# Kernel optimization log

Hardware: AMD Instinct MI355X
Metric: run time of the kernel (lower is better)

## Reference

```python
import jax, jax.numpy as jnp
import numpy as np

B, S, D, DEPTH = 2, 2048, 1024, 4
NUM_LEAVES = 2 ** DEPTH          # 16
NUM_DEC = NUM_LEAVES - 1         # 15


def setup_inputs() -> dict:
    key = jax.random.key(0)
    k1, k2, k3, k4, k5 = jax.random.split(key, 5)
    scale = 1.0 / np.sqrt(D)
    return {
        "x": jax.random.normal(k1, (B, S, D), dtype=jnp.float32),
        "dec_w": jax.random.normal(k2, (NUM_DEC, D), dtype=jnp.float32) * scale,
        "dec_b": jax.random.normal(k3, (NUM_DEC,), dtype=jnp.float32) * scale,
        "leaf_w": jax.random.normal(k4, (NUM_LEAVES, D, D), dtype=jnp.float32) * scale,  # [leaf, out, in] (torch Linear layout)
        "leaf_b": jax.random.normal(k5, (NUM_LEAVES, D), dtype=jnp.float32) * scale,
    }


def reference(x, dec_w, dec_b, leaf_w, leaf_b):
    num_leaves = leaf_w.shape[0]
    num_dec = num_leaves - 1
    # All decision-node sigmoids in one batched GEMM: [B,S,num_dec]
    dec = jax.nn.sigmoid(jnp.einsum("bsd,nd->bsn", x, dec_w) + dec_b)
    # Faithful to the original: each tree slot is multiplied exactly once by its
    # direct parent's decision (left child: p, right child: 1-p).
    leaf_idx = np.arange(num_dec, 2 * num_leaves - 1)      # slots holding leaf probs
    parent = (leaf_idx - 1) // 2                           # [num_leaves]
    is_left = (leaf_idx % 2 == 1)                          # [num_leaves]
    dec_p = dec[..., parent]                               # [B,S,num_leaves]
    leaf_probs = jnp.where(jnp.asarray(is_left), dec_p, 1.0 - dec_p)
    # All leaf MLPs as one batched GEMM: [B,S,L,D]
    leaf_out = jnp.einsum("bsd,lod->bslo", x, leaf_w) + leaf_b
    # Probability-weighted sum over leaves -> [B,S,D]
    return jnp.einsum("bslo,bsl->bso", leaf_out, leaf_probs)
```

## Files before the change

kernel.cpp:

```cpp
#include <hip/hip_runtime.h>
#include <stdint.h>


#define M_TOK 4096
#define DDIM  1024
#define KFLAT 9216

typedef __bf16 bf16x8 __attribute__((ext_vector_type(8)));
typedef float  f32x4  __attribute__((ext_vector_type(4)));
typedef unsigned short u16x4 __attribute__((ext_vector_type(4)));
typedef unsigned short u16x8 __attribute__((ext_vector_type(8)));

#define GLB(p) ((const __attribute__((address_space(1))) void*)(p))
#define LDS(p) ((__attribute__((address_space(3))) void*)(p))

__device__ __forceinline__ unsigned short f2bf(float f) {
    union { float f; uint32_t u; } v; v.f = f;
    uint32_t u = v.u;
    return (unsigned short)((u + 0x7fffu + ((u >> 16) & 1u)) >> 16);
}

__device__ __forceinline__ bf16x8 asbf(f32x4 v) {
    bf16x8 r; __builtin_memcpy(&r, &v, 16); return r;
}

template<int OFF>
__device__ __forceinline__ f32x4 dsr(uint32_t a) {
    f32x4 r;
    asm volatile("ds_read_b128 %0, %1 offset:%c2" : "=v"(r) : "v"(a), "i"(OFF));
    return r;
}

__global__ __launch_bounds__(256) void prep_dec_kernel(
    const float* __restrict__ x, const float* __restrict__ dec_w,
    const float* __restrict__ dec_b, const float* __restrict__ lw,
    const float* __restrict__ lb, unsigned short* __restrict__ wp,
    float* __restrict__ bw, unsigned short* __restrict__ xs,
    float* __restrict__ pmat)
{
    if (blockIdx.x < 1024) {
        int idx = blockIdx.x * 256 + threadIdx.x;
        int o  = idx >> 8;
        int k4 = (idx & 255) << 2;
        size_t src = (size_t)o * DDIM + k4;
        size_t dstb = (size_t)o * KFLAT + k4;
        float4 acc = make_float4(0.f, 0.f, 0.f, 0.f);
#pragma unroll
        for (int j = 0; j < 8; ++j) {
            const float4 a = *(const float4*)(lw + (size_t)(2*j)   * DDIM*DDIM + src);
            const float4 b = *(const float4*)(lw + (size_t)(2*j+1) * DDIM*DDIM + src);
            u16x4 d;
            d[0] = f2bf(a.x - b.x); d[1] = f2bf(a.y - b.y);
            d[2] = f2bf(a.z - b.z); d[3] = f2bf(a.w - b.w);
            *(u16x4*)(wp + dstb + (size_t)j * DDIM) = d;
            acc.x += b.x; acc.y += b.y; acc.z += b.z; acc.w += b.w;
        }
        u16x4 s;
        s[0] = f2bf(acc.x); s[1] = f2bf(acc.y); s[2] = f2bf(acc.z); s[3] = f2bf(acc.w);
        *(u16x4*)(wp + dstb + (size_t)8 * DDIM) = s;
        if ((idx & 255) == 0) {
            float sb = 0.f;
#pragma unroll
            for (int j = 0; j < 8; ++j) {
                float ba = lb[(2*j) * DDIM + o];
                float bb = lb[(2*j+1) * DDIM + o];
                bw[j * DDIM + o] = ba - bb;
                sb += bb;
            }
            bw[8 * DDIM + o] = sb;
        }
    } else {
        int m    = (blockIdx.x - 1024) * 4 + (threadIdx.x >> 6);
        int lane = threadIdx.x & 63;
        const float* xr = x + (size_t)m * DDIM + lane * 16;
        float xv[16];
        *(float4*)&xv[0]  = *(const float4*)(xr + 0);
        *(float4*)&xv[4]  = *(const float4*)(xr + 4);
        *(float4*)&xv[8]  = *(const float4*)(xr + 8);
        *(float4*)&xv[12] = *(const float4*)(xr + 12);
        float s[8];
#pragma unroll
        for (int j = 0; j < 8; ++j) {
            const float* wr = dec_w + (size_t)(7 + j) * DDIM + lane * 16;
            float a = 0.f;
#pragma unroll
            for (int i = 0; i < 16; i += 4) {
                float4 wv = *(const float4*)(wr + i);
                a = fmaf(xv[i], wv.x, fmaf(xv[i+1], wv.y, fmaf(xv[i+2], wv.z, fmaf(xv[i+3], wv.w, a))));
            }
            s[j] = a;
        }
#pragma unroll
        for (int j = 0; j < 8; ++j)
#pragma unroll
            for (int off = 32; off > 0; off >>= 1)
                s[j] += __shfl_xor(s[j], off);
        float p[8];
#pragma unroll
        for (int j = 0; j < 8; ++j)
            p[j] = 1.0f / (1.0f + expf(-(s[j] + dec_b[7 + j])));
        if (lane == 0) {
#pragma unroll
            for (int j = 0; j < 8; ++j)
                pmat[(size_t)m * 8 + j] = p[j];
        }
#pragma unroll
        for (int j = 0; j < 9; ++j) {
            float pj = (j < 8) ? p[j] : 1.0f;
            unsigned short* dst = xs + (size_t)m * KFLAT + j * DDIM + lane * 16;
#pragma unroll
            for (int c = 0; c < 2; ++c) {
                u16x8 o;
#pragma unroll
                for (int e = 0; e < 8; ++e) o[e] = f2bf(pj * xv[c * 8 + e]);
                *(u16x8*)(dst + c * 8) = o;
            }
        }
    }
}

#define WAITV8 asm volatile("s_waitcnt vmcnt(8)" ::: "memory")
#define WAITV4 asm volatile("s_waitcnt vmcnt(4)" ::: "memory")
#define WAITV0 asm volatile("s_waitcnt vmcnt(0)" ::: "memory")
#define BARR   __builtin_amdgcn_s_barrier()
#define LGKM0  do { asm volatile("s_waitcnt lgkmcnt(0)" ::: "memory"); \
                    __builtin_amdgcn_sched_barrier(0); } while(0)
#define LGKM4  do { asm volatile("s_waitcnt lgkmcnt(4)" ::: "memory"); \
                    __builtin_amdgcn_sched_barrier(0); } while(0)

#define MFMA_Q(q, SET) do { \
    __builtin_amdgcn_s_setprio(1); \
    _Pragma("unroll") \
    for (int mfl = 0; mfl < 2; ++mfl) { \
        _Pragma("unroll") \
        for (int j = 0; j < 4; ++j) { \
            acc[2*(q)+mfl][j] = __builtin_amdgcn_mfma_f32_16x16x32_bf16(asbf(SET[mfl][0]), asbf(bv[j][0]), acc[2*(q)+mfl][j], 0, 0, 0); \
            acc[2*(q)+mfl][j] = __builtin_amdgcn_mfma_f32_16x16x32_bf16(asbf(SET[mfl][1]), asbf(bv[j][1]), acc[2*(q)+mfl][j], 0, 0, 0); \
        } \
    } \
    __builtin_amdgcn_s_setprio(0); \
} while(0)

#define READ_A(SET, q) do { \
    SET[0][0] = dsr<(2*(q)+0)*2048>(bA0); \
    SET[0][1] = dsr<(2*(q)+0)*2048>(bA1); \
    SET[1][0] = dsr<(2*(q)+1)*2048>(bA0); \
    SET[1][1] = dsr<(2*(q)+1)*2048>(bA1); \
} while(0)

#define READ_B() do { \
    bv[0][0] = dsr<0*2048>(bB0); bv[0][1] = dsr<0*2048>(bB1); \
    bv[1][0] = dsr<1*2048>(bB0); bv[1][1] = dsr<1*2048>(bB1); \
    bv[2][0] = dsr<2*2048>(bB0); bv[2][1] = dsr<2*2048>(bB1); \
    bv[3][0] = dsr<3*2048>(bB0); bv[3][1] = dsr<3*2048>(bB1); \
} while(0)

__global__ __launch_bounds__(512, 2) void tree_gemm5(
    const unsigned short* __restrict__ xs,
    const unsigned short* __restrict__ wp,
    float* __restrict__ out, float* __restrict__ parts,
    int KG)
{
    extern __shared__ char smem[];
    const int tid  = threadIdx.x;
    const int lane = tid & 63;
    const int w    = tid >> 6;
    const int wm   = w >> 2, wn = w & 3;
    const int ra   = lane & 15;
    const int g16  = lane >> 4;

    const int bx  = blockIdx.x;
    const int xcd = bx & 7, ii = bx >> 3;
    const int nt  = xcd >> 1;
    const int mt  = (xcd & 1) * 8 + ii;
    const int m0  = mt * 256, n0 = nt * 256;
    const int g   = blockIdx.y;
    const int k0  = g * KG;
    const int NT  = KG >> 6;

    uint32_t sbase = (uint32_t)(uintptr_t)(__attribute__((address_space(3))) char*)smem;
    const uint32_t colb0 = (uint32_t)((g16 ^ (ra & 7)) << 4);
    const uint32_t colb1 = colb0 ^ 64;
    const uint32_t baseA0s = sbase + wm * 16384 + ra * 128 + colb0;
    const uint32_t baseA1s = sbase + wm * 16384 + ra * 128 + colb1;
    const uint32_t baseB0s = sbase + 65536 + wn * 8192 + ra * 128 + colb0;
    const uint32_t baseB1s = sbase + 65536 + wn * 8192 + ra * 128 + colb1;

    const int kel = (((lane & 7) ^ (lane >> 3)) & 7) * 8;
    const int rA  = w * 8 + (lane >> 3);

    auto stageA = [&](int buf, int tt, int hh) {
        const unsigned short* s0 = xs + (size_t)(m0 + hh * 128 + rA) * KFLAT + (k0 + tt * 64 + kel);
        char* d0 = smem + buf * 32768 + hh * 16384 + w * 1024;
        __builtin_amdgcn_global_load_lds(GLB(s0), LDS(d0), 16, 0, 0);
        __builtin_amdgcn_global_load_lds(GLB(s0 + (size_t)64 * KFLAT), LDS(d0 + 8192), 16, 0, 0);
    };
    auto stageB = [&](int buf, int tt, int hh) {
        const unsigned short* s0 = wp + (size_t)(n0 + hh * 128 + rA) * KFLAT + (k0 + tt * 64 + kel);
        char* d0 = smem + 65536 + buf * 32768 + hh * 16384 + w * 1024;
        __builtin_amdgcn_global_load_lds(GLB(s0), LDS(d0), 16, 0, 0);
        __builtin_amdgcn_global_load_lds(GLB(s0 + (size_t)64 * KFLAT), LDS(d0 + 8192), 16, 0, 0);
    };

    f32x4 acc[8][4] = {};
    f32x4 avA[2][2], avB[2][2], bv[4][2];

    stageA(0, 0, 0); stageA(0, 0, 1);
    stageB(0, 0, 0); stageB(0, 0, 1);
    stageA(1, 1, 0); stageA(1, 1, 1);
    stageB(1, 1, 0); stageB(1, 1, 1);
    WAITV8;
    BARR;

    int bt = 0, bt2 = 2;
    for (int t = 0; t < NT; ++t) {
        if (t) {
            if (t == NT - 1) { WAITV0; } else { WAITV4; }
            BARR;
        }
        if (t + 1 < NT) { stageA((t + 1) & 1, t + 1, 0); stageA((t + 1) & 1, t + 1, 1); }
        if (t + 2 < NT) { stageB(bt2, t + 2, 0); stageB(bt2, t + 2, 1); }

        const uint32_t aoff = (uint32_t)(t & 1) << 15;
        const uint32_t boff = (uint32_t)bt << 15;
        const uint32_t bA0 = baseA0s + aoff, bA1 = baseA1s + aoff;
        const uint32_t bB0 = baseB0s + boff, bB1 = baseB1s + boff;

        READ_B();
        READ_A(avA, 0);
        READ_A(avB, 1);
        LGKM4;  MFMA_Q(0, avA);
        READ_A(avA, 2);
        LGKM4;  MFMA_Q(1, avB);
        READ_A(avB, 3);
        LGKM4;  MFMA_Q(2, avA);
        LGKM0;  MFMA_Q(3, avB);

        bt  = (bt  == 2) ? 0 : bt  + 1;
        bt2 = (bt2 == 2) ? 0 : bt2 + 1;
    }

    float* dst = (g == 0) ? out : parts + (size_t)(g - 1) * M_TOK * DDIM;
#pragma unroll
    for (int mf = 0; mf < 8; ++mf)
#pragma unroll
        for (int e = 0; e < 4; ++e) {
            int row = m0 + wm * 128 + mf * 16 + g16 * 4 + e;
#pragma unroll
            for (int j = 0; j < 4; ++j)
                dst[(size_t)row * DDIM + n0 + wn * 64 + j * 16 + ra] = acc[mf][j][e];
        }
}

#define READ_AV4(q, b) do { \
    avA[0][0] = dsr<(b)*32768 + (2*(q)+0)*2048>(baseA0); \
    avA[0][1] = dsr<(b)*32768 + (2*(q)+0)*2048>(baseA1); \
    avA[1][0] = dsr<(b)*32768 + (2*(q)+1)*2048>(baseA0); \
    avA[1][1] = dsr<(b)*32768 + (2*(q)+1)*2048>(baseA1); \
} while(0)

#define READ_BV4(b) do { \
    bv[0][0] = dsr<(b)*32768 + 0*2048>(baseB0); bv[0][1] = dsr<(b)*32768 + 0*2048>(baseB1); \
    bv[1][0] = dsr<(b)*32768 + 1*2048>(baseB0); bv[1][1] = dsr<(b)*32768 + 1*2048>(baseB1); \
    bv[2][0] = dsr<(b)*32768 + 2*2048>(baseB0); bv[2][1] = dsr<(b)*32768 + 2*2048>(baseB1); \
    bv[3][0] = dsr<(b)*32768 + 3*2048>(baseB0); bv[3][1] = dsr<(b)*32768 + 3*2048>(baseB1); \
} while(0)

__global__ __launch_bounds__(512, 2) void tree_gemm4(
    const unsigned short* __restrict__ xs, const unsigned short* __restrict__ wp,
    float* __restrict__ out, float* __restrict__ parts, int KG)
{
    extern __shared__ char smem[];
    const int tid  = threadIdx.x;
    const int lane = tid & 63;
    const int w    = tid >> 6;
    const int wm   = w >> 2, wn = w & 3;
    const int ra   = lane & 15;
    const int g16  = lane >> 4;
    const int bx  = blockIdx.x;
    const int xcd = bx & 7, ii = bx >> 3;
    const int nt  = xcd >> 1;
    const int mt  = (xcd & 1) * 8 + ii;
    const int m0  = mt * 256, n0 = nt * 256;
    const int g   = blockIdx.y;
    const int k0  = g * KG;
    const int NI  = KG >> 7;
    uint32_t sbase = (uint32_t)(uintptr_t)(__attribute__((address_space(3))) char*)smem;
    const uint32_t colb0 = (uint32_t)((g16 ^ (ra & 7)) << 4);
    const uint32_t colb1 = colb0 ^ 64;
    const uint32_t baseA0 = sbase + wm * 16384 + ra * 128 + colb0;
    const uint32_t baseA1 = sbase + wm * 16384 + ra * 128 + colb1;
    const uint32_t baseB0 = sbase + 65536 + wn * 8192 + ra * 128 + colb0;
    const uint32_t baseB1 = sbase + 65536 + wn * 8192 + ra * 128 + colb1;
    const int kel = (((lane & 7) ^ (lane >> 3)) & 7) * 8;
    const int rA  = w * 8 + (lane >> 3);
    auto stageA = [&](int buf, int tt, int hh) {
        const unsigned short* s0 = xs + (size_t)(m0 + hh * 128 + rA) * KFLAT + (k0 + tt * 64 + kel);
        char* d0 = smem + buf * 32768 + hh * 16384 + w * 1024;
        __builtin_amdgcn_global_load_lds(GLB(s0), LDS(d0), 16, 0, 0);
        __builtin_amdgcn_global_load_lds(GLB(s0 + (size_t)64 * KFLAT), LDS(d0 + 8192), 16, 0, 0);
    };
    auto stageB = [&](int buf, int tt, int hh) {
        const unsigned short* s0 = wp + (size_t)(n0 + hh * 128 + rA) * KFLAT + (k0 + tt * 64 + kel);
        char* d0 = smem + 65536 + buf * 32768 + hh * 16384 + w * 1024;
        __builtin_amdgcn_global_load_lds(GLB(s0), LDS(d0), 16, 0, 0);
        __builtin_amdgcn_global_load_lds(GLB(s0 + (size_t)64 * KFLAT), LDS(d0 + 8192), 16, 0, 0);
    };
    f32x4 acc[8][4] = {};
    f32x4 avA[2][2], bv[4][2];
    stageA(0, 0, 0); stageA(0, 0, 1);
    stageB(0, 0, 0); stageB(0, 0, 1);
    stageB(1, 1, 0); stageB(1, 1, 1);
    WAITV4; BARR;
    for (int i = 0; i < NI; ++i) {
        const int t = 2 * i;
        const bool on = (i + 1 < NI);
        READ_BV4(0); READ_AV4(0, 0);
        stageA(1, t + 1, 0); stageA(1, t + 1, 1);
        BARR; LGKM0; MFMA_Q(0, avA); BARR;
        READ_AV4(1, 0); if (on) stageB(0, t + 2, 0);
        BARR; LGKM0; MFMA_Q(1, avA); BARR;
        READ_AV4(2, 0); if (on) stageB(0, t + 2, 1);
        BARR; LGKM0; MFMA_Q(2, avA); BARR;
        READ_AV4(3, 0);
        BARR; LGKM0; MFMA_Q(3, avA);
        if (on) { WAITV4; } else { WAITV0; }
        BARR;
        READ_BV4(1); READ_AV4(0, 1);
        if (on) { stageA(0, t + 2, 0); stageA(0, t + 2, 1); }
        BARR; LGKM0; MFMA_Q(0, avA); BARR;
        READ_AV4(1, 1); if (on) stageB(1, t + 3, 0);
        BARR; LGKM0; MFMA_Q(1, avA); BARR;
        READ_AV4(2, 1); if (on) stageB(1, t + 3, 1);
        BARR; LGKM0; MFMA_Q(2, avA); BARR;
        READ_AV4(3, 1);
        BARR; LGKM0; MFMA_Q(3, avA);
        if (on) WAITV4;
        BARR;
    }
    float* dst = (g == 0) ? out : parts + (size_t)(g - 1) * M_TOK * DDIM;
#pragma unroll
    for (int mf = 0; mf < 8; ++mf)
#pragma unroll
        for (int e = 0; e < 4; ++e) {
            int row = m0 + wm * 128 + mf * 16 + g16 * 4 + e;
#pragma unroll
            for (int j = 0; j < 4; ++j)
                dst[(size_t)row * DDIM + n0 + wn * 64 + j * 16 + ra] = acc[mf][j][e];
        }
}

__global__ __launch_bounds__(256) void reduce2_kernel(
    float* __restrict__ out, const float* __restrict__ parts,
    const float* __restrict__ pmat, const float* __restrict__ bw, int np)
{
    size_t i = (size_t)blockIdx.x * 256 + threadIdx.x;
    int m   = (int)(i >> 8);
    int col = (int)(i & 255) * 4;
    float4 a = ((const float4*)out)[i];
    for (int p = 0; p < np; ++p) {
        float4 b = ((const float4*)(parts + (size_t)p * M_TOK * DDIM))[i];
        a.x += b.x; a.y += b.y; a.z += b.z; a.w += b.w;
    }
    float4 pa = *(const float4*)(pmat + (size_t)m * 8);
    float4 pb = *(const float4*)(pmat + (size_t)m * 8 + 4);
    float4 bias = *(const float4*)(bw + 8 * DDIM + col);
#pragma unroll
    for (int l = 0; l < 8; ++l) {
        float pl = (l < 4) ? ((const float*)&pa)[l] : ((const float*)&pb)[l - 4];
        float4 bl = *(const float4*)(bw + l * DDIM + col);
        bias.x = fmaf(pl, bl.x, bias.x); bias.y = fmaf(pl, bl.y, bias.y);
        bias.z = fmaf(pl, bl.z, bias.z); bias.w = fmaf(pl, bl.w, bias.w);
    }
    a.x += bias.x; a.y += bias.y; a.z += bias.z; a.w += bias.w;
    ((float4*)out)[i] = a;
}

__global__ __launch_bounds__(256, 4) void tree_gemm3(
    const unsigned short* __restrict__ xs, const unsigned short* __restrict__ wp,
    const float* __restrict__ bw, const float* __restrict__ pmat,
    float* __restrict__ out, float* __restrict__ parts, int KG)
{
    __shared__ __align__(16) unsigned short Asm[2][128 * 32];
    __shared__ __align__(16) unsigned short Bsm[2][128 * 32];
    const int tid  = threadIdx.x;
    const int lane = tid & 63;
    const int w    = tid >> 6;
    const int wm   = w >> 1, wn = w & 1;
    const int bx   = blockIdx.x;
    const int xcd  = bx & 7;
    const int ii   = bx >> 3;
    const int mt   = xcd * 4 + (ii >> 3);
    const int nt   = ii & 7;
    const int m0   = mt * 128, n0 = nt * 128;
    const int g    = blockIdx.y;
    const int k0   = g * KG;
    const int ra   = lane & 15;
    const int kb   = (lane >> 4) * 8;
    f32x4 acc[4][4] = {};
    auto stage = [&](int buf, int t) {
#pragma unroll
        for (int c = 0; c < 2; ++c) {
            int row = w * 32 + c * 16 + (lane >> 2);
            int ke  = k0 + t * 32 + (lane & 3) * 8;
            const unsigned short* ga = xs + (size_t)(m0 + row) * KFLAT + ke;
            __builtin_amdgcn_global_load_lds(GLB(ga), LDS(&Asm[buf][w * 1024 + c * 512]), 16, 0, 0);
            const unsigned short* gb = wp + (size_t)(n0 + row) * KFLAT + ke;
            __builtin_amdgcn_global_load_lds(GLB(gb), LDS(&Bsm[buf][w * 1024 + c * 512]), 16, 0, 0);
// ... 58 lines not shown
{
    size_t i = (size_t)blockIdx.x * 256 + threadIdx.x;
    float4 a = ((const float4*)out)[i];
    for (int p = 0; p < np; ++p) {
        float4 b = ((const float4*)(parts + (size_t)p * M_TOK * DDIM))[i];
        a.x += b.x; a.y += b.y; a.z += b.z; a.w += b.w;
    }
    ((float4*)out)[i] = a;
}

extern "C" void kernel_launch(void* const* d_in, const int* in_sizes, int n_in,
                              void* d_out, int out_size, void* d_ws, size_t ws_size,
                              hipStream_t stream) {
    (void)in_sizes; (void)n_in; (void)out_size;
    const float* x     = (const float*)d_in[0];
    const float* dec_w = (const float*)d_in[1];
    const float* dec_b = (const float*)d_in[2];
    const float* lw    = (const float*)d_in[3];
    const float* lb    = (const float*)d_in[4];
    float* out = (float*)d_out;
    uint8_t* w8 = (uint8_t*)d_ws;

    unsigned short* xs   = (unsigned short*)(w8);
    unsigned short* wp   = (unsigned short*)(w8 + 75497472);
    float*          bw   = (float*)(w8 + 94371840);
    float*          pmat = (float*)(w8 + 94408704);
    float*          parts= (float*)(w8 + 94539776);
    const size_t NEED3 = 94539776 + 2ull * 16777216;
    const size_t NEED4 = 94539776 + 3ull * 16777216;

    int ks = (ws_size >= NEED4) ? 4 : (ws_size >= NEED3) ? 3 : 0;
    if (!ks) return;

    prep_dec_kernel<<<2048, 256, 0, stream>>>(x, dec_w, dec_b, lw, lb, wp, bw, xs, pmat);

    hipError_t e5 = hipFuncSetAttribute(
        reinterpret_cast<const void*>(tree_gemm5),
        hipFuncAttributeMaxDynamicSharedMemorySize, 163840);
    if (e5 == hipSuccess) {
        tree_gemm5<<<dim3(64, ks), 512, 163840, stream>>>(xs, wp, out, parts, KFLAT / ks);
        reduce2_kernel<<<4096, 256, 0, stream>>>(out, parts, pmat, bw, ks - 1);
        return;
    }
    hipError_t e4 = hipFuncSetAttribute(
        reinterpret_cast<const void*>(tree_gemm4),
        hipFuncAttributeMaxDynamicSharedMemorySize, 131072);
    if (e4 == hipSuccess) {
        tree_gemm4<<<dim3(64, ks), 512, 131072, stream>>>(xs, wp, out, parts, KFLAT / ks);
        reduce2_kernel<<<4096, 256, 0, stream>>>(out, parts, pmat, bw, ks - 1);
    } else {
        tree_gemm3<<<dim3(256, ks), 256, 0, stream>>>(xs, wp, bw, pmat, out, parts, KFLAT / ks);
        reduce_kernel<<<4096, 256, 0, stream>>>(out, parts, ks - 1);
    }
}
```

Baseline: 126.2 us.

## Pre-swizzle weights into MFMA fragment layout and load B directly to registers

The weight-prep kernel now writes the bf16 weight matrix in a tiled layout that matches the per-lane MFMA B-fragment order. A new GEMM kernel reads B fragments straight from global memory into registers instead of staging them through LDS. This cuts LDS use to 64KB per block, which may allow more blocks per CU. The grid is remapped to 256 flat blocks with a fixed 4-way K split and XCD-aware tile assignment. The cost is that B loads are no longer shared across the waves of a block, so there is more global or L2 traffic and exposed load latency, and the A pipeline is reduced to a double buffer.

```diff
diff --git a/kernel.cpp b/kernel.cpp
--- a/kernel.cpp
+++ b/kernel.cpp
@@ -36,14 +36,28 @@
     const float* __restrict__ dec_b, const float* __restrict__ lw,
     const float* __restrict__ lb, unsigned short* __restrict__ wp,
     float* __restrict__ bw, unsigned short* __restrict__ xs,
-    float* __restrict__ pmat)
+    float* __restrict__ pmat, int newlay)
 {
     if (blockIdx.x < 1024) {
         int idx = blockIdx.x * 256 + threadIdx.x;
         int o  = idx >> 8;
         int k4 = (idx & 255) << 2;
         size_t src = (size_t)o * DDIM + k4;
-        size_t dstb = (size_t)o * KFLAT + k4;
+        const int nt = o >> 8, wn = (o >> 6) & 3, jj = (o >> 4) & 3, ra = o & 15;
+        auto store4 = [&](int l, u16x4 d) {
+            if (newlay) {
+                int K    = l * DDIM + k4;
+                int kt   = K >> 6;
+                int half = (K >> 5) & 1;
+                int g16  = (K >> 3) & 3;
+                int e0   = K & 7;
+                size_t a = ((size_t)(nt * 144 + kt) * 4 + wn) * 4096
+                         + (jj * 2 + half) * 512 + (g16 * 16 + ra) * 8 + e0;
+                *(u16x4*)(wp + a) = d;
+            } else {
+                *(u16x4*)(wp + (size_t)o * KFLAT + l * DDIM + k4) = d;
+            }
+        };
         float4 acc = make_float4(0.f, 0.f, 0.f, 0.f);
 #pragma unroll
         for (int j = 0; j < 8; ++j) {
@@ -52,12 +66,12 @@
             u16x4 d;
             d[0] = f2bf(a.x - b.x); d[1] = f2bf(a.y - b.y);
             d[2] = f2bf(a.z - b.z); d[3] = f2bf(a.w - b.w);
-            *(u16x4*)(wp + dstb + (size_t)j * DDIM) = d;
+            store4(j, d);
             acc.x += b.x; acc.y += b.y; acc.z += b.z; acc.w += b.w;
         }
         u16x4 s;
         s[0] = f2bf(acc.x); s[1] = f2bf(acc.y); s[2] = f2bf(acc.z); s[3] = f2bf(acc.w);
-        *(u16x4*)(wp + dstb + (size_t)8 * DDIM) = s;
+        store4(8, s);
         if ((idx & 255) == 0) {
             float sb = 0.f;
 #pragma unroll
@@ -119,14 +133,16 @@
     }
 }
 
-#define WAITV8 asm volatile("s_waitcnt vmcnt(8)" ::: "memory")
-#define WAITV4 asm volatile("s_waitcnt vmcnt(4)" ::: "memory")
 #define WAITV0 asm volatile("s_waitcnt vmcnt(0)" ::: "memory")
 #define BARR   __builtin_amdgcn_s_barrier()
 #define LGKM0  do { asm volatile("s_waitcnt lgkmcnt(0)" ::: "memory"); \
                     __builtin_amdgcn_sched_barrier(0); } while(0)
 #define LGKM4  do { asm volatile("s_waitcnt lgkmcnt(4)" ::: "memory"); \
                     __builtin_amdgcn_sched_barrier(0); } while(0)
+#define WAITV4LG4 do { asm volatile("s_waitcnt vmcnt(4) lgkmcnt(4)" ::: "memory"); \
+                       __builtin_amdgcn_sched_barrier(0); } while(0)
+#define WAITV0LG4 do { asm volatile("s_waitcnt vmcnt(0) lgkmcnt(4)" ::: "memory"); \
+                       __builtin_amdgcn_sched_barrier(0); } while(0)
 
 #define MFMA_Q(q, SET) do { \
     __builtin_amdgcn_s_setprio(1); \
@@ -141,25 +157,17 @@
     __builtin_amdgcn_s_setprio(0); \
 } while(0)
 
-#define READ_A(SET, q) do { \
-    SET[0][0] = dsr<(2*(q)+0)*2048>(bA0); \
-    SET[0][1] = dsr<(2*(q)+0)*2048>(bA1); \
-    SET[1][0] = dsr<(2*(q)+1)*2048>(bA0); \
-    SET[1][1] = dsr<(2*(q)+1)*2048>(bA1); \
+#define RD_A(SET, q, boff) do { \
+    SET[0][0] = dsr<(2*(q)+0)*2048>(bA0 + (boff)); \
+    SET[0][1] = dsr<(2*(q)+0)*2048>(bA1 + (boff)); \
+    SET[1][0] = dsr<(2*(q)+1)*2048>(bA0 + (boff)); \
+    SET[1][1] = dsr<(2*(q)+1)*2048>(bA1 + (boff)); \
 } while(0)
 
-#define READ_B() do { \
-    bv[0][0] = dsr<0*2048>(bB0); bv[0][1] = dsr<0*2048>(bB1); \
-    bv[1][0] = dsr<1*2048>(bB0); bv[1][1] = dsr<1*2048>(bB1); \
-    bv[2][0] = dsr<2*2048>(bB0); bv[2][1] = dsr<2*2048>(bB1); \
-    bv[3][0] = dsr<3*2048>(bB0); bv[3][1] = dsr<3*2048>(bB1); \
-} while(0)
-
-__global__ __launch_bounds__(512, 2) void tree_gemm5(
+__global__ __launch_bounds__(512, 2) void tree_gemm6(
     const unsigned short* __restrict__ xs,
-    const unsigned short* __restrict__ wp,
-    float* __restrict__ out, float* __restrict__ parts,
-    int KG)
+    const unsigned short* __restrict__ wpf,
+    float* __restrict__ out, float* __restrict__ parts)
 {
     extern __shared__ char smem[];
     const int tid  = threadIdx.x;
@@ -169,22 +177,23 @@
     const int ra   = lane & 15;
     const int g16  = lane >> 4;
 
-    const int bx  = blockIdx.x;
-    const int xcd = bx & 7, ii = bx >> 3;
-    const int nt  = xcd >> 1;
-    const int mt  = (xcd & 1) * 8 + ii;
-    const int m0  = mt * 256, n0 = nt * 256;
-    const int g   = blockIdx.y;
-    const int k0  = g * KG;
-    const int NT  = KG >> 6;
+    const int flat = blockIdx.x;
+    const int xcd  = flat & 7;
+    const int idx  = flat >> 3;
+    const int cc   = idx >> 4;
+    const int mt   = idx & 15;
+    const int code = xcd * 2 + cc;
+    const int nt   = code >> 2;
+    const int g    = code & 3;
+    const int m0   = mt * 256, n0 = nt * 256;
+    const int k0   = g * 2304;
+    const int NT   = 36;
 
     uint32_t sbase = (uint32_t)(uintptr_t)(__attribute__((address_space(3))) char*)smem;
     const uint32_t colb0 = (uint32_t)((g16 ^ (ra & 7)) << 4);
     const uint32_t colb1 = colb0 ^ 64;
-    const uint32_t baseA0s = sbase + wm * 16384 + ra * 128 + colb0;
-    const uint32_t baseA1s = sbase + wm * 16384 + ra * 128 + colb1;
-    const uint32_t baseB0s = sbase + 65536 + wn * 8192 + ra * 128 + colb0;
-    const uint32_t baseB1s = sbase + 65536 + wn * 8192 + ra * 128 + colb1;
+    const uint32_t bA0 = sbase + wm * 16384 + ra * 128 + colb0;
+    const uint32_t bA1 = sbase + wm * 16384 + ra * 128 + colb1;
 
     const int kel = (((lane & 7) ^ (lane >> 3)) & 7) * 8;
     const int rA  = w * 8 + (lane >> 3);
@@ -195,49 +204,39 @@
         __builtin_amdgcn_global_load_lds(GLB(s0), LDS(d0), 16, 0, 0);
         __builtin_amdgcn_global_load_lds(GLB(s0 + (size_t)64 * KFLAT), LDS(d0 + 8192), 16, 0, 0);
     };
-    auto stageB = [&](int buf, int tt, int hh) {
-        const unsigned short* s0 = wp + (size_t)(n0 + hh * 128 + rA) * KFLAT + (k0 + tt * 64 + kel);
-        char* d0 = smem + 65536 + buf * 32768 + hh * 16384 + w * 1024;
-        __builtin_amdgcn_global_load_lds(GLB(s0), LDS(d0), 16, 0, 0);
-        __builtin_amdgcn_global_load_lds(GLB(s0 + (size_t)64 * KFLAT), LDS(d0 + 8192), 16, 0, 0);
-    };
+
+    const unsigned short* bsrc = wpf
+        + ((size_t)(nt * 144 + g * 36) * 4 + wn) * 4096 + lane * 8;
 
     f32x4 acc[8][4] = {};
     f32x4 avA[2][2], avB[2][2], bv[4][2];
 
     stageA(0, 0, 0); stageA(0, 0, 1);
-    stageB(0, 0, 0); stageB(0, 0, 1);
-    stageA(1, 1, 0); stageA(1, 1, 1);
-    stageB(1, 1, 0); stageB(1, 1, 1);
-    WAITV8;
+    WAITV0;
     BARR;
 
-    int bt = 0, bt2 = 2;
     for (int t = 0; t < NT; ++t) {
-        if (t) {
-            if (t == NT - 1) { WAITV0; } else { WAITV4; }
-            BARR;
-        }
-        if (t + 1 < NT) { stageA((t + 1) & 1, t + 1, 0); stageA((t + 1) & 1, t + 1, 1); }
-        if (t + 2 < NT) { stageB(bt2, t + 2, 0); stageB(bt2, t + 2, 1); }
-
-        const uint32_t aoff = (uint32_t)(t & 1) << 15;
-        const uint32_t boff = (uint32_t)bt << 15;
-        const uint32_t bA0 = baseA0s + aoff, bA1 = baseA1s + aoff;
-        const uint32_t bB0 = baseB0s + boff, bB1 = baseB1s + boff;
-
-        READ_B();
-        READ_A(avA, 0);
-        READ_A(avB, 1);
-        LGKM4;  MFMA_Q(0, avA);
-        READ_A(avA, 2);
+        const bool on = (t + 1 < NT);
+#pragma unroll
+        for (int j = 0; j < 4; ++j) {
+            bv[j][0] = *(const f32x4*)(bsrc + (j * 2 + 0) * 512);
+            bv[j][1] = *(const f32x4*)(bsrc + (j * 2 + 1) * 512);
+        }
+        if (on) { stageA((t + 1) & 1, t + 1, 0); stageA((t + 1) & 1, t + 1, 1); }
+
+        const uint32_t boff = (uint32_t)(t & 1) << 15;
+        RD_A(avA, 0, boff);
+        RD_A(avB, 1, boff);
+        if (on) { WAITV4LG4; } else { WAITV0LG4; }
+        MFMA_Q(0, avA);
+        RD_A(avA, 2, boff);
         LGKM4;  MFMA_Q(1, avB);
-        READ_A(avB, 3);
+        RD_A(avB, 3, boff);
         LGKM4;  MFMA_Q(2, avA);
         LGKM0;  MFMA_Q(3, avB);
 
-        bt  = (bt  == 2) ? 0 : bt  + 1;
-        bt2 = (bt2 == 2) ? 0 : bt2 + 1;
+        if (on) { WAITV0; BARR; }
+        bsrc += 16384;
     }
 
     float* dst = (g == 0) ? out : parts + (size_t)(g - 1) * M_TOK * DDIM;
@@ -252,21 +251,48 @@
         }
 }
 
-#define READ_AV4(q, b) do { \
-    avA[0][0] = dsr<(b)*32768 + (2*(q)+0)*2048>(baseA0); \
-    avA[0][1] = dsr<(b)*32768 + (2*(q)+0)*2048>(baseA1); \
-    avA[1][0] = dsr<(b)*32768 + (2*(q)+1)*2048>(baseA0); \
-    avA[1][1] = dsr<(b)*32768 + (2*(q)+1)*2048>(baseA1); \
+__global__ __launch_bounds__(256) void reduce2_kernel(
+    float* __restrict__ out, const float* __restrict__ parts,
+    const float* __restrict__ pmat, const float* __restrict__ bw, int np)
+{
+    size_t i = (size_t)blockIdx.x * 256 + threadIdx.x;
+    int m   = (int)(i >> 8);
+    int col = (int)(i & 255) * 4;
+    float4 a = ((const float4*)out)[i];
+    for (int p = 0; p < np; ++p) {
+        float4 b = ((const float4*)(parts + (size_t)p * M_TOK * DDIM))[i];
+        a.x += b.x; a.y += b.y; a.z += b.z; a.w += b.w;
+    }
+    float4 pa = *(const float4*)(pmat + (size_t)m * 8);
+    float4 pb = *(const float4*)(pmat + (size_t)m * 8 + 4);
+    float4 bias = *(const float4*)(bw + 8 * DDIM + col);
+#pragma unroll
+    for (int l = 0; l < 8; ++l) {
+        float pl = (l < 4) ? ((const float*)&pa)[l] : ((const float*)&pb)[l - 4];
+        float4 bl = *(const float4*)(bw + l * DDIM + col);
+        bias.x = fmaf(pl, bl.x, bias.x); bias.y = fmaf(pl, bl.y, bias.y);
+        bias.z = fmaf(pl, bl.z, bias.z); bias.w = fmaf(pl, bl.w, bias.w);
+    }
+    a.x += bias.x; a.y += bias.y; a.z += bias.z; a.w += bias.w;
+    ((float4*)out)[i] = a;
+}
+
+#define READ_A5(SET, q) do { \
+    SET[0][0] = dsr<(2*(q)+0)*2048>(bA0); \
+    SET[0][1] = dsr<(2*(q)+0)*2048>(bA1); \
+    SET[1][0] = dsr<(2*(q)+1)*2048>(bA0); \
+    SET[1][1] = dsr<(2*(q)+1)*2048>(bA1); \
 } while(0)
-
-#define READ_BV4(b) do { \
-    bv[0][0] = dsr<(b)*32768 + 0*2048>(baseB0); bv[0][1] = dsr<(b)*32768 + 0*2048>(baseB1); \
-    bv[1][0] = dsr<(b)*32768 + 1*2048>(baseB0); bv[1][1] = dsr<(b)*32768 + 1*2048>(baseB1); \
-    bv[2][0] = dsr<(b)*32768 + 2*2048>(baseB0); bv[2][1] = dsr<(b)*32768 + 2*2048>(baseB1); \
-    bv[3][0] = dsr<(b)*32768 + 3*2048>(baseB0); bv[3][1] = dsr<(b)*32768 + 3*2048>(baseB1); \
+#define READ_B5() do { \
+    bv[0][0] = dsr<0*2048>(bB0); bv[0][1] = dsr<0*2048>(bB1); \
+    bv[1][0] = dsr<1*2048>(bB0); bv[1][1] = dsr<1*2048>(bB1); \
+    bv[2][0] = dsr<2*2048>(bB0); bv[2][1] = dsr<2*2048>(bB1); \
+    bv[3][0] = dsr<3*2048>(bB0); bv[3][1] = dsr<3*2048>(bB1); \
 } while(0)
-
-__global__ __launch_bounds__(512, 2) void tree_gemm4(
+#define WAITV8 asm volatile("s_waitcnt vmcnt(8)" ::: "memory")
+#define WAITV4 asm volatile("s_waitcnt vmcnt(4)" ::: "memory")
+
+__global__ __launch_bounds__(512, 2) void tree_gemm5(
     const unsigned short* __restrict__ xs, const unsigned short* __restrict__ wp,
     float* __restrict__ out, float* __restrict__ parts, int KG)
 {
@@ -284,14 +310,14 @@
     const int m0  = mt * 256, n0 = nt * 256;
     const int g   = blockIdx.y;
     const int k0  = g * KG;
-    const int NI  = KG >> 7;
+    const int NT  = KG >> 6;
     uint32_t sbase = (uint32_t)(uintptr_t)(__attribute__((address_space(3))) char*)smem;
     const uint32_t colb0 = (uint32_t)((g16 ^ (ra & 7)) << 4);
     const uint32_t colb1 = colb0 ^ 64;
-    const uint32_t baseA0 = sbase + wm * 16384 + ra * 128 + colb0;
-    const uint32_t baseA1 = sbase + wm * 16384 + ra * 128 + colb1;
-    const uint32_t baseB0 = sbase + 65536 + wn * 8192 + ra * 128 + colb0;
-    const uint32_t baseB1 = sbase + 65536 + wn * 8192 + ra * 128 + colb1;
+    const uint32_t baseA0s = sbase + wm * 16384 + ra * 128 + colb0;
+    const uint32_t baseA1s = sbase + wm * 16384 + ra * 128 + colb1;
+    const uint32_t baseB0s = sbase + 65536 + wn * 8192 + ra * 128 + colb0;
+    const uint32_t baseB1s = sbase + 65536 + wn * 8192 + ra * 128 + colb1;
     const int kel = (((lane & 7) ^ (lane >> 3)) & 7) * 8;
     const int rA  = w * 8 + (lane >> 3);
     auto stageA = [&](int buf, int tt, int hh) {
@@ -307,36 +333,35 @@
         __builtin_amdgcn_global_load_lds(GLB(s0 + (size_t)64 * KFLAT), LDS(d0 + 8192), 16, 0, 0);
     };
     f32x4 acc[8][4] = {};
-    f32x4 avA[2][2], bv[4][2];
+    f32x4 avA[2][2], avB[2][2], bv[4][2];
     stageA(0, 0, 0); stageA(0, 0, 1);
     stageB(0, 0, 0); stageB(0, 0, 1);
+    stageA(1, 1, 0); stageA(1, 1, 1);
     stageB(1, 1, 0); stageB(1, 1, 1);
-    WAITV4; BARR;
-    for (int i = 0; i < NI; ++i) {
-        const int t = 2 * i;
-        const bool on = (i + 1 < NI);
-        READ_BV4(0); READ_AV4(0, 0);
-        stageA(1, t + 1, 0); stageA(1, t + 1, 1);
-        BARR; LGKM0; MFMA_Q(0, avA); BARR;
-        READ_AV4(1, 0); if (on) stageB(0, t + 2, 0);
-        BARR; LGKM0; MFMA_Q(1, avA); BARR;
-        READ_AV4(2, 0); if (on) stageB(0, t + 2, 1);
-        BARR; LGKM0; MFMA_Q(2, avA); BARR;
-        READ_AV4(3, 0);
-        BARR; LGKM0; MFMA_Q(3, avA);
-        if (on) { WAITV4; } else { WAITV0; }
-        BARR;
-        READ_BV4(1); READ_AV4(0, 1);
-        if (on) { stageA(0, t + 2, 0); stageA(0, t + 2, 1); }
-        BARR; LGKM0; MFMA_Q(0, avA); BARR;
-        READ_AV4(1, 1); if (on) stageB(1, t + 3, 0);
-        BARR; LGKM0; MFMA_Q(1, avA); BARR;
-        READ_AV4(2, 1); if (on) stageB(1, t + 3, 1);
-        BARR; LGKM0; MFMA_Q(2, avA); BARR;
-        READ_AV4(3, 1);
-        BARR; LGKM0; MFMA_Q(3, avA);
-        if (on) WAITV4;
-        BARR;
+    WAITV8; BARR;
+    int bt = 0, bt2 = 2;
+    for (int t = 0; t < NT; ++t) {
+        if (t) {
+            if (t == NT - 1) { WAITV0; } else { WAITV4; }
+            BARR;
+        }
+        if (t + 1 < NT) { stageA((t + 1) & 1, t + 1, 0); stageA((t + 1) & 1, t + 1, 1); }
+        if (t + 2 < NT) { stageB(bt2, t + 2, 0); stageB(bt2, t + 2, 1); }
+        const uint32_t aoff = (uint32_t)(t & 1) << 15;
+        const uint32_t boffv = (uint32_t)bt << 15;
+        const uint32_t bA0 = baseA0s + aoff, bA1 = baseA1s + aoff;
+        const uint32_t bB0 = baseB0s + boffv, bB1 = baseB1s + boffv;
+        READ_B5();
+        READ_A5(avA, 0);
+        READ_A5(avB, 1);
+        LGKM4;  MFMA_Q(0, avA);
+        READ_A5(avA, 2);
+        LGKM4;  MFMA_Q(1, avB);
+        READ_A5(avB, 3);
+        LGKM4;  MFMA_Q(2, avA);
+        LGKM0;  MFMA_Q(3, avB);
+        bt  = (bt  == 2) ? 0 : bt  + 1;
+        bt2 = (bt2 == 2) ? 0 : bt2 + 1;
     }
     float* dst = (g == 0) ? out : parts + (size_t)(g - 1) * M_TOK * DDIM;
 #pragma unroll
@@ -348,32 +373,6 @@
             for (int j = 0; j < 4; ++j)
                 dst[(size_t)row * DDIM + n0 + wn * 64 + j * 16 + ra] = acc[mf][j][e];
         }
-}
-
-__global__ __launch_bounds__(256) void reduce2_kernel(
-    float* __restrict__ out, const float* __restrict__ parts,
-    const float* __restrict__ pmat, const float* __restrict__ bw, int np)
-{
-    size_t i = (size_t)blockIdx.x * 256 + threadIdx.x;
-    int m   = (int)(i >> 8);
-    int col = (int)(i & 255) * 4;
-    float4 a = ((const float4*)out)[i];
-    for (int p = 0; p < np; ++p) {
-        float4 b = ((const float4*)(parts + (size_t)p * M_TOK * DDIM))[i];
-        a.x += b.x; a.y += b.y; a.z += b.z; a.w += b.w;
-    }
-    float4 pa = *(const float4*)(pmat + (size_t)m * 8);
-    float4 pb = *(const float4*)(pmat + (size_t)m * 8 + 4);
-    float4 bias = *(const float4*)(bw + 8 * DDIM + col);
-#pragma unroll
-    for (int l = 0; l < 8; ++l) {
-        float pl = (l < 4) ? ((const float*)&pa)[l] : ((const float*)&pb)[l - 4];
-        float4 bl = *(const float4*)(bw + l * DDIM + col);
-        bias.x = fmaf(pl, bl.x, bias.x); bias.y = fmaf(pl, bl.y, bias.y);
-        bias.z = fmaf(pl, bl.z, bias.z); bias.w = fmaf(pl, bl.w, bias.w);
-    }
-    a.x += bias.x; a.y += bias.y; a.z += bias.z; a.w += bias.w;
-    ((float4*)out)[i] = a;
 }
 
 __global__ __launch_bounds__(256, 4) void tree_gemm3(
@@ -498,7 +497,22 @@
     int ks = (ws_size >= NEED4) ? 4 : (ws_size >= NEED3) ? 3 : 0;
     if (!ks) return;
 
-    prep_dec_kernel<<<2048, 256, 0, stream>>>(x, dec_w, dec_b, lw, lb, wp, bw, xs, pmat);
+    bool use6 = false;
+    if (ks == 4) {
+        hipError_t e6 = hipFuncSetAttribute(
+            reinterpret_cast<const void*>(tree_gemm6),
+            hipFuncAttributeMaxDynamicSharedMemorySize, 65536);
+        use6 = (e6 == hipSuccess);
+    }
+
+    prep_dec_kernel<<<2048, 256, 0, stream>>>(x, dec_w, dec_b, lw, lb, wp, bw, xs, pmat,
+                                              use6 ? 1 : 0);
+
+    if (use6) {
+        tree_gemm6<<<256, 512, 65536, stream>>>(xs, wp, out, parts);
+        reduce2_kernel<<<4096, 256, 0, stream>>>(out, parts, pmat, bw, 3);
+        return;
+    }
 
     hipError_t e5 = hipFuncSetAttribute(
         reinterpret_cast<const void*>(tree_gemm5),
@@ -506,14 +520,6 @@
     if (e5 == hipSuccess) {
         tree_gemm5<<<dim3(64, ks), 512, 163840, stream>>>(xs, wp, out, parts, KFLAT / ks);
         reduce2_kernel<<<4096, 256, 0, stream>>>(out, parts, pmat, bw, ks - 1);
-        return;
-    }
-    hipError_t e4 = hipFuncSetAttribute(
-        reinterpret_cast<const void*>(tree_gemm4),
-        hipFuncAttributeMaxDynamicSharedMemorySize, 131072);
-    if (e4 == hipSuccess) {
-        tree_gemm4<<<dim3(64, ks), 512, 131072, stream>>>(xs, wp, out, parts, KFLAT / ks);
-        reduce2_kernel<<<4096, 256, 0, stream>>>(out, parts, pmat, bw, ks - 1);
     } else {
         tree_gemm3<<<dim3(256, ks), 256, 0, stream>>>(xs, wp, bw, pmat, out, parts, KFLAT / ks);
         reduce_kernel<<<4096, 256, 0, stream>>>(out, parts, ks - 1);
```

Measured after the change: 141.8 us. 1.12x slower.

## Prefetch next tile's LDS fragments before last MFMA quarter with double-buffered B registers

Applied to the files above, without the earlier changes.

Adds a tree_gemm8 kernel that software-pipelines the LDS-to-register reads. It issues the barrier and the next tile's B and A-quarter-0 reads before the final MFMA quarter of the current tile, and ping-pongs between two B register sets. The unroll-by-two loop hides LDS read latency at tile boundaries, which the old per-tile barrier-then-read sequence exposed. It costs more VGPRs and adds a loop that assumes NT is even; the old tree_gemm4 fallback is removed.

```diff
diff --git a/kernel.cpp b/kernel.cpp
--- a/kernel.cpp
+++ b/kernel.cpp
@@ -119,47 +119,44 @@
     }
 }
 
+#define WAITV0 asm volatile("s_waitcnt vmcnt(0)" ::: "memory")
+#define WAITV4 asm volatile("s_waitcnt vmcnt(4)" ::: "memory")
 #define WAITV8 asm volatile("s_waitcnt vmcnt(8)" ::: "memory")
-#define WAITV4 asm volatile("s_waitcnt vmcnt(4)" ::: "memory")
-#define WAITV0 asm volatile("s_waitcnt vmcnt(0)" ::: "memory")
 #define BARR   __builtin_amdgcn_s_barrier()
-#define LGKM0  do { asm volatile("s_waitcnt lgkmcnt(0)" ::: "memory"); \
-                    __builtin_amdgcn_sched_barrier(0); } while(0)
-#define LGKM4  do { asm volatile("s_waitcnt lgkmcnt(4)" ::: "memory"); \
-                    __builtin_amdgcn_sched_barrier(0); } while(0)
-
-#define MFMA_Q(q, SET) do { \
+#define SBAR   __builtin_amdgcn_sched_barrier(0)
+#define LGKM0  do { asm volatile("s_waitcnt lgkmcnt(0)" ::: "memory"); SBAR; } while(0)
+#define LGKM4  do { asm volatile("s_waitcnt lgkmcnt(4)" ::: "memory"); SBAR; } while(0)
+
+#define MFMA_Q(q, ASET, BSET) do { \
     __builtin_amdgcn_s_setprio(1); \
     _Pragma("unroll") \
     for (int mfl = 0; mfl < 2; ++mfl) { \
         _Pragma("unroll") \
         for (int j = 0; j < 4; ++j) { \
-            acc[2*(q)+mfl][j] = __builtin_amdgcn_mfma_f32_16x16x32_bf16(asbf(SET[mfl][0]), asbf(bv[j][0]), acc[2*(q)+mfl][j], 0, 0, 0); \
-            acc[2*(q)+mfl][j] = __builtin_amdgcn_mfma_f32_16x16x32_bf16(asbf(SET[mfl][1]), asbf(bv[j][1]), acc[2*(q)+mfl][j], 0, 0, 0); \
+            acc[2*(q)+mfl][j] = __builtin_amdgcn_mfma_f32_16x16x32_bf16(asbf(ASET[mfl][0]), asbf(BSET[j][0]), acc[2*(q)+mfl][j], 0, 0, 0); \
+            acc[2*(q)+mfl][j] = __builtin_amdgcn_mfma_f32_16x16x32_bf16(asbf(ASET[mfl][1]), asbf(BSET[j][1]), acc[2*(q)+mfl][j], 0, 0, 0); \
         } \
     } \
     __builtin_amdgcn_s_setprio(0); \
 } while(0)
 
-#define READ_A(SET, q) do { \
-    SET[0][0] = dsr<(2*(q)+0)*2048>(bA0); \
-    SET[0][1] = dsr<(2*(q)+0)*2048>(bA1); \
-    SET[1][0] = dsr<(2*(q)+1)*2048>(bA0); \
-    SET[1][1] = dsr<(2*(q)+1)*2048>(bA1); \
+#define READ_A(SET, q, a0, a1) do { \
+    SET[0][0] = dsr<(2*(q)+0)*2048>(a0); \
+    SET[0][1] = dsr<(2*(q)+0)*2048>(a1); \
+    SET[1][0] = dsr<(2*(q)+1)*2048>(a0); \
+    SET[1][1] = dsr<(2*(q)+1)*2048>(a1); \
 } while(0)
 
-#define READ_B() do { \
-    bv[0][0] = dsr<0*2048>(bB0); bv[0][1] = dsr<0*2048>(bB1); \
-    bv[1][0] = dsr<1*2048>(bB0); bv[1][1] = dsr<1*2048>(bB1); \
-    bv[2][0] = dsr<2*2048>(bB0); bv[2][1] = dsr<2*2048>(bB1); \
-    bv[3][0] = dsr<3*2048>(bB0); bv[3][1] = dsr<3*2048>(bB1); \
+#define READ_B(SET, b0, b1) do { \
+    SET[0][0] = dsr<0*2048>(b0); SET[0][1] = dsr<0*2048>(b1); \
+    SET[1][0] = dsr<1*2048>(b0); SET[1][1] = dsr<1*2048>(b1); \
+    SET[2][0] = dsr<2*2048>(b0); SET[2][1] = dsr<2*2048>(b1); \
+    SET[3][0] = dsr<3*2048>(b0); SET[3][1] = dsr<3*2048>(b1); \
 } while(0)
 
-__global__ __launch_bounds__(512, 2) void tree_gemm5(
-    const unsigned short* __restrict__ xs,
-    const unsigned short* __restrict__ wp,
-    float* __restrict__ out, float* __restrict__ parts,
-    int KG)
+__global__ __launch_bounds__(512, 2) void tree_gemm8(
+    const unsigned short* __restrict__ xs, const unsigned short* __restrict__ wp,
+    float* __restrict__ out, float* __restrict__ parts, int KG)
 {
     extern __shared__ char smem[];
     const int tid  = threadIdx.x;
@@ -203,42 +200,53 @@
     };
 
     f32x4 acc[8][4] = {};
-    f32x4 avA[2][2], avB[2][2], bv[4][2];
+    f32x4 avA[2][2], avB[2][2], bvX[4][2], bvY[4][2];
 
     stageA(0, 0, 0); stageA(0, 0, 1);
     stageB(0, 0, 0); stageB(0, 0, 1);
-    stageA(1, 1, 0); stageA(1, 1, 1);
     stageB(1, 1, 0); stageB(1, 1, 1);
-    WAITV8;
+    WAITV4;
     BARR;
-
-    int bt = 0, bt2 = 2;
-    for (int t = 0; t < NT; ++t) {
-        if (t) {
-            if (t == NT - 1) { WAITV0; } else { WAITV4; }
-            BARR;
-        }
-        if (t + 1 < NT) { stageA((t + 1) & 1, t + 1, 0); stageA((t + 1) & 1, t + 1, 1); }
-        if (t + 2 < NT) { stageB(bt2, t + 2, 0); stageB(bt2, t + 2, 1); }
-
-        const uint32_t aoff = (uint32_t)(t & 1) << 15;
-        const uint32_t boff = (uint32_t)bt << 15;
-        const uint32_t bA0 = baseA0s + aoff, bA1 = baseA1s + aoff;
-        const uint32_t bB0 = baseB0s + boff, bB1 = baseB1s + boff;
-
-        READ_B();
-        READ_A(avA, 0);
-        READ_A(avB, 1);
-        LGKM4;  MFMA_Q(0, avA);
-        READ_A(avA, 2);
-        LGKM4;  MFMA_Q(1, avB);
-        READ_A(avB, 3);
-        LGKM4;  MFMA_Q(2, avA);
-        LGKM0;  MFMA_Q(3, avB);
-
-        bt  = (bt  == 2) ? 0 : bt  + 1;
-        bt2 = (bt2 == 2) ? 0 : bt2 + 1;
-    }
+    READ_B(bvX, baseB0s, baseB1s);
+    READ_A(avA, 0, baseA0s, baseA1s);
+
+    int bt1 = 1, bt2 = 2;
+
+#define TILE_BODY(T, CUR, NXT) do { \
+    const int t_ = (T); \
+    const bool s1 = (t_ + 1 < NT), s2 = (t_ + 2 < NT); \
+    if (s1) { stageA((t_ + 1) & 1, t_ + 1, 0); stageA((t_ + 1) & 1, t_ + 1, 1); } \
+    if (s2) { stageB(bt2, t_ + 2, 0); stageB(bt2, t_ + 2, 1); } \
+    const uint32_t a0_ = baseA0s + ((uint32_t)(t_ & 1) << 15); \
+    const uint32_t a1_ = baseA1s + ((uint32_t)(t_ & 1) << 15); \
+    READ_A(avB, 1, a0_, a1_); \
+    LGKM4;  MFMA_Q(0, avA, CUR); \
+    READ_A(avA, 2, a0_, a1_); \
+    LGKM4;  MFMA_Q(1, avB, CUR); \
+    READ_A(avB, 3, a0_, a1_); \
+    LGKM4;  MFMA_Q(2, avA, CUR); \
+    LGKM0; \
+    if (s1) { \
+        if (s2) { WAITV4; } else { WAITV0; } \
+        BARR; \
+        const uint32_t nb0_ = baseB0s + (uint32_t)bt1 * 32768u; \
+        const uint32_t nb1_ = baseB1s + (uint32_t)bt1 * 32768u; \
+        const uint32_t na0_ = baseA0s + ((uint32_t)((t_ + 1) & 1) << 15); \
+        const uint32_t na1_ = baseA1s + ((uint32_t)((t_ + 1) & 1) << 15); \
+        READ_B(NXT, nb0_, nb1_); \
+        READ_A(avA, 0, na0_, na1_); \
+    } \
+    MFMA_Q(3, avB, CUR); \
+    SBAR; \
+    bt1 = (bt1 == 2) ? 0 : bt1 + 1; \
+    bt2 = (bt2 == 2) ? 0 : bt2 + 1; \
+} while(0)
+
+    for (int tp = 0; tp < NT; tp += 2) {
+        TILE_BODY(tp,     bvX, bvY);
+        TILE_BODY(tp + 1, bvY, bvX);
+    }
+#undef TILE_BODY
 
     float* dst = (g == 0) ? out : parts + (size_t)(g - 1) * M_TOK * DDIM;
 #pragma unroll
@@ -252,21 +260,46 @@
         }
 }
 
-#define READ_AV4(q, b) do { \
-    avA[0][0] = dsr<(b)*32768 + (2*(q)+0)*2048>(baseA0); \
-    avA[0][1] = dsr<(b)*32768 + (2*(q)+0)*2048>(baseA1); \
-    avA[1][0] = dsr<(b)*32768 + (2*(q)+1)*2048>(baseA0); \
-    avA[1][1] = dsr<(b)*32768 + (2*(q)+1)*2048>(baseA1); \
+__global__ __launch_bounds__(256) void reduce2_kernel(
+    float* __restrict__ out, const float* __restrict__ parts,
+    const float* __restrict__ pmat, const float* __restrict__ bw, int np)
+{
+    size_t i = (size_t)blockIdx.x * 256 + threadIdx.x;
+    int m   = (int)(i >> 8);
+    int col = (int)(i & 255) * 4;
+    float4 a = ((const float4*)out)[i];
+    for (int p = 0; p < np; ++p) {
+        float4 b = ((const float4*)(parts + (size_t)p * M_TOK * DDIM))[i];
+        a.x += b.x; a.y += b.y; a.z += b.z; a.w += b.w;
+    }
+    float4 pa = *(const float4*)(pmat + (size_t)m * 8);
+    float4 pb = *(const float4*)(pmat + (size_t)m * 8 + 4);
+    float4 bias = *(const float4*)(bw + 8 * DDIM + col);
+#pragma unroll
+    for (int l = 0; l < 8; ++l) {
+        float pl = (l < 4) ? ((const float*)&pa)[l] : ((const float*)&pb)[l - 4];
+        float4 bl = *(const float4*)(bw + l * DDIM + col);
+        bias.x = fmaf(pl, bl.x, bias.x); bias.y = fmaf(pl, bl.y, bias.y);
+        bias.z = fmaf(pl, bl.z, bias.z); bias.w = fmaf(pl, bl.w, bias.w);
+    }
+    a.x += bias.x; a.y += bias.y; a.z += bias.z; a.w += bias.w;
+    ((float4*)out)[i] = a;
+}
+
+#define MFMA_Q5(q, SET) do { \
+    __builtin_amdgcn_s_setprio(1); \
+    _Pragma("unroll") \
+    for (int mfl = 0; mfl < 2; ++mfl) { \
+        _Pragma("unroll") \
+        for (int j = 0; j < 4; ++j) { \
+            acc[2*(q)+mfl][j] = __builtin_amdgcn_mfma_f32_16x16x32_bf16(asbf(SET[mfl][0]), asbf(bv[j][0]), acc[2*(q)+mfl][j], 0, 0, 0); \
+            acc[2*(q)+mfl][j] = __builtin_amdgcn_mfma_f32_16x16x32_bf16(asbf(SET[mfl][1]), asbf(bv[j][1]), acc[2*(q)+mfl][j], 0, 0, 0); \
+        } \
+    } \
+    __builtin_amdgcn_s_setprio(0); \
 } while(0)
 
-#define READ_BV4(b) do { \
-    bv[0][0] = dsr<(b)*32768 + 0*2048>(baseB0); bv[0][1] = dsr<(b)*32768 + 0*2048>(baseB1); \
-    bv[1][0] = dsr<(b)*32768 + 1*2048>(baseB0); bv[1][1] = dsr<(b)*32768 + 1*2048>(baseB1); \
-    bv[2][0] = dsr<(b)*32768 + 2*2048>(baseB0); bv[2][1] = dsr<(b)*32768 + 2*2048>(baseB1); \
-    bv[3][0] = dsr<(b)*32768 + 3*2048>(baseB0); bv[3][1] = dsr<(b)*32768 + 3*2048>(baseB1); \
-} while(0)
-
-__global__ __launch_bounds__(512, 2) void tree_gemm4(
+__global__ __launch_bounds__(512, 2) void tree_gemm5(
     const unsigned short* __restrict__ xs, const unsigned short* __restrict__ wp,
     float* __restrict__ out, float* __restrict__ parts, int KG)
 {
@@ -284,14 +317,14 @@
     const int m0  = mt * 256, n0 = nt * 256;
     const int g   = blockIdx.y;
     const int k0  = g * KG;
-    const int NI  = KG >> 7;
+    const int NT  = KG >> 6;
     uint32_t sbase = (uint32_t)(uintptr_t)(__attribute__((address_space(3))) char*)smem;
     const uint32_t colb0 = (uint32_t)((g16 ^ (ra & 7)) << 4);
     const uint32_t colb1 = colb0 ^ 64;
-    const uint32_t baseA0 = sbase + wm * 16384 + ra * 128 + colb0;
-    const uint32_t baseA1 = sbase + wm * 16384 + ra * 128 + colb1;
-    const uint32_t baseB0 = sbase + 65536 + wn * 8192 + ra * 128 + colb0;
-    const uint32_t baseB1 = sbase + 65536 + wn * 8192 + ra * 128 + colb1;
+    const uint32_t baseA0s = sbase + wm * 16384 + ra * 128 + colb0;
+    const uint32_t baseA1s = sbase + wm * 16384 + ra * 128 + colb1;
+    const uint32_t baseB0s = sbase + 65536 + wn * 8192 + ra * 128 + colb0;
+    const uint32_t baseB1s = sbase + 65536 + wn * 8192 + ra * 128 + colb1;
     const int kel = (((lane & 7) ^ (lane >> 3)) & 7) * 8;
     const int rA  = w * 8 + (lane >> 3);
     auto stageA = [&](int buf, int tt, int hh) {
@@ -307,36 +340,35 @@
         __builtin_amdgcn_global_load_lds(GLB(s0 + (size_t)64 * KFLAT), LDS(d0 + 8192), 16, 0, 0);
     };
     f32x4 acc[8][4] = {};
-    f32x4 avA[2][2], bv[4][2];
+    f32x4 avA[2][2], avB[2][2], bv[4][2];
     stageA(0, 0, 0); stageA(0, 0, 1);
     stageB(0, 0, 0); stageB(0, 0, 1);
+    stageA(1, 1, 0); stageA(1, 1, 1);
     stageB(1, 1, 0); stageB(1, 1, 1);
-    WAITV4; BARR;
-    for (int i = 0; i < NI; ++i) {
-        const int t = 2 * i;
-        const bool on = (i + 1 < NI);
-        READ_BV4(0); READ_AV4(0, 0);
-        stageA(1, t + 1, 0); stageA(1, t + 1, 1);
-        BARR; LGKM0; MFMA_Q(0, avA); BARR;
-        READ_AV4(1, 0); if (on) stageB(0, t + 2, 0);
-        BARR; LGKM0; MFMA_Q(1, avA); BARR;
-        READ_AV4(2, 0); if (on) stageB(0, t + 2, 1);
-        BARR; LGKM0; MFMA_Q(2, avA); BARR;
-        READ_AV4(3, 0);
-        BARR; LGKM0; MFMA_Q(3, avA);
-        if (on) { WAITV4; } else { WAITV0; }
-        BARR;
-        READ_BV4(1); READ_AV4(0, 1);
-        if (on) { stageA(0, t + 2, 0); stageA(0, t + 2, 1); }
-        BARR; LGKM0; MFMA_Q(0, avA); BARR;
-        READ_AV4(1, 1); if (on) stageB(1, t + 3, 0);
-        BARR; LGKM0; MFMA_Q(1, avA); BARR;
-        READ_AV4(2, 1); if (on) stageB(1, t + 3, 1);
-        BARR; LGKM0; MFMA_Q(2, avA); BARR;
-        READ_AV4(3, 1);
-        BARR; LGKM0; MFMA_Q(3, avA);
-        if (on) WAITV4;
-        BARR;
+    WAITV8; BARR;
+    int bt = 0, bt2 = 2;
+    for (int t = 0; t < NT; ++t) {
+        if (t) {
+            if (t == NT - 1) { WAITV0; } else { WAITV4; }
+            BARR;
+        }
+        if (t + 1 < NT) { stageA((t + 1) & 1, t + 1, 0); stageA((t + 1) & 1, t + 1, 1); }
+        if (t + 2 < NT) { stageB(bt2, t + 2, 0); stageB(bt2, t + 2, 1); }
+        const uint32_t aoff = (uint32_t)(t & 1) << 15;
+        const uint32_t boffv = (uint32_t)bt << 15;
+        const uint32_t bA0 = baseA0s + aoff, bA1 = baseA1s + aoff;
+        const uint32_t bB0 = baseB0s + boffv, bB1 = baseB1s + boffv;
+        READ_B(bv, bB0, bB1);
+        READ_A(avA, 0, bA0, bA1);
+        READ_A(avB, 1, bA0, bA1);
+        LGKM4;  MFMA_Q5(0, avA);
+        READ_A(avA, 2, bA0, bA1);
+        LGKM4;  MFMA_Q5(1, avB);
+        READ_A(avB, 3, bA0, bA1);
+        LGKM4;  MFMA_Q5(2, avA);
+        LGKM0;  MFMA_Q5(3, avB);
+        bt  = (bt  == 2) ? 0 : bt  + 1;
+        bt2 = (bt2 == 2) ? 0 : bt2 + 1;
     }
     float* dst = (g == 0) ? out : parts + (size_t)(g - 1) * M_TOK * DDIM;
 #pragma unroll
@@ -348,32 +380,6 @@
             for (int j = 0; j < 4; ++j)
                 dst[(size_t)row * DDIM + n0 + wn * 64 + j * 16 + ra] = acc[mf][j][e];
         }
-}
-
-__global__ __launch_bounds__(256) void reduce2_kernel(
-    float* __restrict__ out, const float* __restrict__ parts,
-    const float* __restrict__ pmat, const float* __restrict__ bw, int np)
-{
-    size_t i = (size_t)blockIdx.x * 256 + threadIdx.x;
-    int m   = (int)(i >> 8);
-    int col = (int)(i & 255) * 4;
-    float4 a = ((const float4*)out)[i];
-    for (int p = 0; p < np; ++p) {
-        float4 b = ((const float4*)(parts + (size_t)p * M_TOK * DDIM))[i];
-        a.x += b.x; a.y += b.y; a.z += b.z; a.w += b.w;
-    }
-    float4 pa = *(const float4*)(pmat + (size_t)m * 8);
-    float4 pb = *(const float4*)(pmat + (size_t)m * 8 + 4);
-    float4 bias = *(const float4*)(bw + 8 * DDIM + col);
-#pragma unroll
-    for (int l = 0; l < 8; ++l) {
-        float pl = (l < 4) ? ((const float*)&pa)[l] : ((const float*)&pb)[l - 4];
-        float4 bl = *(const float4*)(bw + l * DDIM + col);
-        bias.x = fmaf(pl, bl.x, bias.x); bias.y = fmaf(pl, bl.y, bias.y);
-        bias.z = fmaf(pl, bl.z, bias.z); bias.w = fmaf(pl, bl.w, bias.w);
-    }
-    a.x += bias.x; a.y += bias.y; a.z += bias.z; a.w += bias.w;
-    ((float4*)out)[i] = a;
 }
 
 __global__ __launch_bounds__(256, 4) void tree_gemm3(
@@ -500,20 +506,20 @@
 
     prep_dec_kernel<<<2048, 256, 0, stream>>>(x, dec_w, dec_b, lw, lb, wp, bw, xs, pmat);
 
+    hipError_t e8 = hipFuncSetAttribute(
+        reinterpret_cast<const void*>(tree_gemm8),
+        hipFuncAttributeMaxDynamicSharedMemorySize, 163840);
+    if (e8 == hipSuccess) {
+        tree_gemm8<<<dim3(64, ks), 512, 163840, stream>>>(xs, wp, out, parts, KFLAT / ks);
+        reduce2_kernel<<<4096, 256, 0, stream>>>(out, parts, pmat, bw, ks - 1);
+        return;
+    }
     hipError_t e5 = hipFuncSetAttribute(
         reinterpret_cast<const void*>(tree_gemm5),
         hipFuncAttributeMaxDynamicSharedMemorySize, 163840);
     if (e5 == hipSuccess) {
         tree_gemm5<<<dim3(64, ks), 512, 163840, stream>>>(xs, wp, out, parts, KFLAT / ks);
         reduce2_kernel<<<4096, 256, 0, stream>>>(out, parts, pmat, bw, ks - 1);
-        return;
-    }
-    hipError_t e4 = hipFuncSetAttribute(
-        reinterpret_cast<const void*>(tree_gemm4),
-        hipFuncAttributeMaxDynamicSharedMemorySize, 131072);
-    if (e4 == hipSuccess) {
-        tree_gemm4<<<dim3(64, ks), 512, 131072, stream>>>(xs, wp, out, parts, KFLAT / ks);
-        reduce2_kernel<<<4096, 256, 0, stream>>>(out, parts, pmat, bw, ks - 1);
     } else {
         tree_gemm3<<<dim3(256, ks), 256, 0, stream>>>(xs, wp, bw, pmat, out, parts, KFLAT / ks);
         reduce_kernel<<<4096, 256, 0, stream>>>(out, parts, ks - 1);
```

New measurement: 123.4 us. -2.2%, faster.
